# Kernel tuning notes

Hardware: AMD Instinct MI355X
Metric: run time of the kernel (lower is better)

Reference implementation:

```python
import jax, jax.numpy as jnp
import numpy as np

TOP_K = 2


def setup_inputs() -> dict:
    key = jax.random.key(0)
    k1, k2, k3, k4 = jax.random.split(key, 4)
    B, D, H, E = 16384, 1024, 1024, 8
    return {
        "x": jax.random.normal(k1, (B, D), dtype=jnp.float32),
        "Wv": jax.random.normal(k2, (E, D, H), dtype=jnp.float32),
        "Wg": jax.random.normal(k3, (E, D, H), dtype=jnp.float32),
        "gate_w": jax.random.normal(k4, (E, D), dtype=jnp.float32) * (1.0 / np.sqrt(D)),
        "gate_b": jnp.zeros((E,), dtype=jnp.float32),
    }


def reference(x, Wv, Wg, gate_w, gate_b):
    # Router: softmax over expert logits, then top-k selection.
    logits = x @ gate_w.T + gate_b                      # [B, E]
    probs = jax.nn.softmax(logits, axis=1)
    topk_scores, topk_idx = jax.lax.top_k(probs, TOP_K)  # [B, K]

    B, E = probs.shape
    # Scatter top-k scores into a dense [B, E] combine matrix (zeros elsewhere).
    combine = jnp.zeros((B, E), dtype=probs.dtype).at[
        jnp.arange(B)[:, None], topk_idx
    ].add(topk_scores)

    # Dense per-expert SwiGLU; combine matrix zeros out non-selected experts,
    # so the math matches the grouped-gemm top-k dispatch exactly.
    v = jnp.einsum("bd,edh->beh", x, Wv)                # [B, E, H]
    g = jnp.einsum("bd,edh->beh", x, Wg)                # [B, E, H]
    act = v * jax.nn.sigmoid(g)                         # SwiGLU-style gating
    return jnp.einsum("be,beh->bh", combine, act)       # weighted combine [B, H]
```

## Files before the change

### kernel.cpp

```cpp
#include <hip/hip_runtime.h>

#define D_DIM 1024
#define H_DIM 1024
#define E_NUM 8
#define BM 128
#define BN 128
#define BK 64
#define CAP 5120
#define RT_TOK 32

typedef __attribute__((ext_vector_type(8))) _Float16 h8v;
typedef __attribute__((ext_vector_type(4))) _Float16 h4v;
typedef __attribute__((ext_vector_type(4))) float f4v;

__device__ __forceinline__ unsigned short f2h(float f) {
  union { _Float16 h; unsigned short u; } c;
  c.h = (_Float16)f;
  return c.u;
}

__global__ void convert_x_kernel(const float4* __restrict__ x,
                                 unsigned short* __restrict__ xh, int n4) {
  int i = blockIdx.x * blockDim.x + threadIdx.x;
  if (i >= n4) return;
  float4 v = x[i];
  ushort4 o;
  o.x = f2h(v.x); o.y = f2h(v.y); o.z = f2h(v.z); o.w = f2h(v.w);
  *(ushort4*)(xh + (size_t)i * 4) = o;
}

__global__ void transpose_w_kernel(const float* __restrict__ W,
                                   unsigned short* __restrict__ Wt) {
  __shared__ float tile[32][33];
  int e = blockIdx.z;
  int h0 = blockIdx.x * 32, d0 = blockIdx.y * 32;
  const float* Wp = W + (size_t)e * D_DIM * H_DIM;
  unsigned short* Wtp = Wt + (size_t)e * H_DIM * D_DIM;
#pragma unroll
  for (int j = 0; j < 32; j += 8)
    tile[threadIdx.y + j][threadIdx.x] =
        Wp[(size_t)(d0 + threadIdx.y + j) * H_DIM + (h0 + threadIdx.x)];
  __syncthreads();
#pragma unroll
  for (int j = 0; j < 32; j += 8)
    Wtp[(size_t)(h0 + threadIdx.y + j) * D_DIM + (d0 + threadIdx.x)] =
        f2h(tile[threadIdx.x][threadIdx.y + j]);
}

__global__ __launch_bounds__(256) void router_kernel(
    const float4* __restrict__ x4, const float4* __restrict__ gw4,
    const float* __restrict__ gb, int* __restrict__ counts,
    int* __restrict__ bucket, float* __restrict__ scoreB,
    int* __restrict__ slotOf, int B) {
  __shared__ float4 gwS[E_NUM * 256];
  __shared__ short eSelS[RT_TOK][2];
  __shared__ float sSelS[RT_TOK][2];
  __shared__ int lCnt[E_NUM], lBase[E_NUM];
  __shared__ unsigned char lOff[RT_TOK][2];
  int tid = threadIdx.x;
  for (int i = tid; i < E_NUM * 256; i += 256) gwS[i] = gw4[i];
  if (tid < E_NUM) lCnt[tid] = 0;
  __syncthreads();
  int wid = tid >> 6, lane = tid & 63;
  for (int rep = 0; rep < RT_TOK / 4; rep++) {
    int t = wid * (RT_TOK / 4) + rep;
    int b = blockIdx.x * RT_TOK + t;
    float acc[E_NUM];
#pragma unroll
    for (int e = 0; e < E_NUM; e++) acc[e] = 0.0f;
#pragma unroll
    for (int i = 0; i < 4; i++) {
      float4 xv = x4[(size_t)b * 256 + i * 64 + lane];
#pragma unroll
      for (int e = 0; e < E_NUM; e++) {
        float4 w = gwS[e * 256 + i * 64 + lane];
        acc[e] += xv.x * w.x + xv.y * w.y + xv.z * w.z + xv.w * w.w;
      }
    }
#pragma unroll
    for (int e = 0; e < E_NUM; e++) {
#pragma unroll
      for (int off = 32; off > 0; off >>= 1) acc[e] += __shfl_down(acc[e], off);
    }
    if (lane == 0) {
      float l[E_NUM];
#pragma unroll
      for (int e = 0; e < E_NUM; e++) l[e] = acc[e] + gb[e];
      int i0 = 0;
#pragma unroll
      for (int e = 1; e < E_NUM; e++) if (l[e] > l[i0]) i0 = e;
      int i1 = (i0 == 0) ? 1 : 0;
#pragma unroll
      for (int e = 0; e < E_NUM; e++) if (e != i0 && l[e] > l[i1]) i1 = e;
      float mx = l[i0];
      float denom = 0.0f;
#pragma unroll
      for (int e = 0; e < E_NUM; e++) denom += __expf(l[e] - mx);
      eSelS[t][0] = (short)i0; sSelS[t][0] = 1.0f / denom;
      eSelS[t][1] = (short)i1; sSelS[t][1] = __expf(l[i1] - mx) / denom;
    }
  }
  __syncthreads();
  if (tid < RT_TOK) {
    lOff[tid][0] = (unsigned char)atomicAdd(&lCnt[eSelS[tid][0]], 1);
    lOff[tid][1] = (unsigned char)atomicAdd(&lCnt[eSelS[tid][1]], 1);
  }
  __syncthreads();
  if (tid < E_NUM) lBase[tid] = atomicAdd(&counts[tid * 32], lCnt[tid]);
  __syncthreads();
  if (tid < RT_TOK) {
    int b = blockIdx.x * RT_TOK + tid;
#pragma unroll
    for (int j = 0; j < 2; j++) {
      int e = eSelS[tid][j];
      int pos = lBase[e] + lOff[tid][j];
      if (pos < CAP) {
        int slot = e * CAP + pos;
        bucket[slot] = b;
        scoreB[slot] = sSelS[tid][j];
        slotOf[b * 2 + j] = slot;
      }
    }
  }
}

template <bool USE_PARTIAL>
__global__ __launch_bounds__(256, 2) void moe_gemm_kernel(
    const unsigned short* __restrict__ xh, const unsigned short* __restrict__ Wvt,
    const unsigned short* __restrict__ Wgt, const int* __restrict__ counts,
    const int* __restrict__ bucket, const float* __restrict__ scoreB,
    _Float16* __restrict__ partial, float* __restrict__ out, int B) {
  int e = blockIdx.z;
  int cnt = counts[e * 32];
  int m0 = blockIdx.x * BM;
  if (m0 >= cnt) return;
  int n0 = blockIdx.y * BN;

  __shared__ unsigned short As[BM * BK];
  __shared__ unsigned short Bvs[BN * BK];
  __shared__ unsigned short Bgs[BN * BK];
  __shared__ int tokS[BM];
  __shared__ float scS[BM];

  int tid = threadIdx.x;
  if (tid < BM) {
    int gr = m0 + tid;
    bool vld = gr < cnt;
    tokS[tid] = vld ? bucket[e * CAP + gr] : 0;
    scS[tid] = vld ? scoreB[e * CAP + gr] : 0.0f;
  }
  __syncthreads();

  int wid = tid >> 6, lane = tid & 63;
  int wm = wid & 1, wn = wid >> 1;
  int quad = lane >> 4, lr = lane & 15;

  f4v accv[4][4], accg[4][4];
#pragma unroll
  for (int a = 0; a < 4; a++)
#pragma unroll
    for (int bb = 0; bb < 4; bb++) {
      f4v z = {0.f, 0.f, 0.f, 0.f};
      accv[a][bb] = z;
      accg[a][bb] = z;
    }

  const unsigned short* Bv0 = Wvt + (size_t)(e * H_DIM + n0) * D_DIM;
  const unsigned short* Bg0 = Wgt + (size_t)(e * H_DIM + n0) * D_DIM;

  for (int kt = 0; kt < D_DIM / BK; kt++) {
    int k0 = kt * BK;
    uint4 va[4], vb[4], vg[4];
#pragma unroll
    for (int i = 0; i < 4; i++) {
      int id = tid + 256 * i;
      int row = id >> 3, c = id & 7;
      int tok = tokS[row];
      va[i] = *(const uint4*)(xh + (size_t)tok * D_DIM + k0 + c * 8);
      vb[i] = *(const uint4*)(Bv0 + (size_t)row * D_DIM + k0 + c * 8);
      vg[i] = *(const uint4*)(Bg0 + (size_t)row * D_DIM + k0 + c * 8);
    }
#pragma unroll
    for (int i = 0; i < 4; i++) {
      int id = tid + 256 * i;
      int row = id >> 3, c = id & 7;
      int off = row * BK + ((c ^ (row & 7)) * 8);
      *(uint4*)(As + off) = va[i];
      *(uint4*)(Bvs + off) = vb[i];
      *(uint4*)(Bgs + off) = vg[i];
    }
    __syncthreads();

    h8v af[4][2], bfr[4][2];
#pragma unroll
    for (int fm = 0; fm < 4; fm++)
#pragma unroll
      for (int s = 0; s < 2; s++) {
        int row = wm * 64 + fm * 16 + lr;
        int c = s * 4 + quad;
        af[fm][s] = *(const h8v*)(As + row * BK + ((c ^ (row & 7)) * 8));
      }
#pragma unroll
    for (int fn = 0; fn < 4; fn++)
#pragma unroll
      for (int s = 0; s < 2; s++) {
        int row = wn * 64 + fn * 16 + lr;
        int c = s * 4 + quad;
        bfr[fn][s] = *(const h8v*)(Bvs + row * BK + ((c ^ (row & 7)) * 8));
      }
#pragma unroll
    for (int fm = 0; fm < 4; fm++)
#pragma unroll
      for (int fn = 0; fn < 4; fn++)
#pragma unroll
        for (int s = 0; s < 2; s++)
          accv[fm][fn] = __builtin_amdgcn_mfma_f32_16x16x32_f16(
              af[fm][s], bfr[fn][s], accv[fm][fn], 0, 0, 0);
#pragma unroll
    for (int fn = 0; fn < 4; fn++)
#pragma unroll
      for (int s = 0; s < 2; s++) {
        int row = wn * 64 + fn * 16 + lr;
        int c = s * 4 + quad;
        bfr[fn][s] = *(const h8v*)(Bgs + row * BK + ((c ^ (row & 7)) * 8));
      }
#pragma unroll
    for (int fm = 0; fm < 4; fm++)
#pragma unroll
      for (int fn = 0; fn < 4; fn++)
#pragma unroll
        for (int s = 0; s < 2; s++)
          accg[fm][fn] = __builtin_amdgcn_mfma_f32_16x16x32_f16(
              af[fm][s], bfr[fn][s], accg[fm][fn], 0, 0, 0);
    __syncthreads();
  }

#pragma unroll
  for (int fm = 0; fm < 4; fm++) {
#pragma unroll
    for (int r = 0; r < 4; r++) {
      int row = wm * 64 + fm * 16 + quad * 4 + r;
      float sc = scS[row];
      if (USE_PARTIAL) {
        int slot = e * CAP + m0 + row;
        _Float16* pr = partial + (size_t)slot * H_DIM;
#pragma unroll
        for (int fn = 0; fn < 4; fn++) {
          int col = n0 + wn * 64 + fn * 16 + lr;
          float v = accv[fm][fn][r];
          float g = accg[fm][fn][r];
          pr[col] = (_Float16)(v * sc / (1.0f + __expf(-g)));
        }
      } else {
        int tok = tokS[row];
#pragma unroll
        for (int fn = 0; fn < 4; fn++) {
          int col = n0 + wn * 64 + fn * 16 + lr;
          float v = accv[fm][fn][r];
          float g = accg[fm][fn][r];
          atomicAdd(&out[(size_t)tok * H_DIM + col], v * sc / (1.0f + __expf(-g)));
        }
      }
    }
  }
}

__global__ __launch_bounds__(256) void gather_kernel(
    const _Float16* __restrict__ partial, const int* __restrict__ slotOf,
    float* __restrict__ out) {
  int b = blockIdx.x;
  int tid = threadIdx.x;
  int s0 = slotOf[b * 2], s1 = slotOf[b * 2 + 1];
  h4v a = ((const h4v*)(partial + (size_t)s0 * H_DIM))[tid];
  h4v c = ((const h4v*)(partial + (size_t)s1 * H_DIM))[tid];
  float4 o;
  o.x = (float)a[0] + (float)c[0];
  o.y = (float)a[1] + (float)c[1];
  o.z = (float)a[2] + (float)c[2];
  o.w = (float)a[3] + (float)c[3];
  ((float4*)(out + (size_t)b * H_DIM))[tid] = o;
}

extern "C" void kernel_launch(void* const* d_in, const int* in_sizes, int n_in,
                              void* d_out, int out_size, void* d_ws, size_t ws_size,
                              hipStream_t stream) {
  const float* x = (const float*)d_in[0];
  const float* Wv = (const float*)d_in[1];
  const float* Wg = (const float*)d_in[2];
  const float* gw = (const float*)d_in[3];
  const float* gb = (const float*)d_in[4];
  float* out = (float*)d_out;
  const int B = in_sizes[0] / D_DIM;

  char* ws = (char*)d_ws;
  unsigned short* xh = (unsigned short*)ws;
  size_t off = (size_t)B * D_DIM * 2;
  unsigned short* Wvt = (unsigned short*)(ws + off);
  off += (size_t)E_NUM * H_DIM * D_DIM * 2;
  unsigned short* Wgt = (unsigned short*)(ws + off);
  off += (size_t)E_NUM * H_DIM * D_DIM * 2;
  int* counts = (int*)(ws + off);
  off += 4096;
  int* bucket = (int*)(ws + off);
  off += (size_t)E_NUM * CAP * 4;
  float* scoreB = (float*)(ws + off);
  off += (size_t)E_NUM * CAP * 4;
  int* slotOf = (int*)(ws + off);
  off += (size_t)B * 2 * 4;
  _Float16* partial = (_Float16*)(ws + off);
  size_t need = off + (size_t)E_NUM * CAP * H_DIM * 2;
  bool use_partial = ws_size >= need;

  hipMemsetAsync(counts, 0, 4096, stream);
  if (!use_partial) hipMemsetAsync(d_out, 0, (size_t)out_size * 4, stream);

  int n4 = B * D_DIM / 4;
  convert_x_kernel<<<(n4 + 255) / 256, 256, 0, stream>>>((const float4*)x, xh, n4);
  transpose_w_kernel<<<dim3(H_DIM / 32, D_DIM / 32, E_NUM), dim3(32, 8), 0, stream>>>(Wv, Wvt);
  transpose_w_kernel<<<dim3(H_DIM / 32, D_DIM / 32, E_NUM), dim3(32, 8), 0, stream>>>(Wg, Wgt);
  router_kernel<<<B / RT_TOK, 256, 0, stream>>>(
      (const float4*)x, (const float4*)gw, gb, counts, bucket, scoreB, slotOf, B);
  if (use_partial) {
    moe_gemm_kernel<true><<<dim3(CAP / BM, H_DIM / BN, E_NUM), 256, 0, stream>>>(
        xh, Wvt, Wgt, counts, bucket, scoreB, partial, out, B);
    gather_kernel<<<B, 256, 0, stream>>>(partial, slotOf, out);
  } else {
    moe_gemm_kernel<false><<<dim3(CAP / BM, H_DIM / BN, E_NUM), 256, 0, stream>>>(
        xh, Wvt, Wgt, counts, bucket, scoreB, partial, out, B);
  }
}
```

Measured before the change: 390.6 us.

## Fuse x conversion into router, use direct global-to-LDS loads, widen transpose and gather

Measured after the change: 355.9 us. 8.9% less time.

```diff
diff --git a/kernel.cpp b/kernel.cpp
--- a/kernel.cpp
+++ b/kernel.cpp
@@ -10,7 +10,6 @@
 #define RT_TOK 32
 
 typedef __attribute__((ext_vector_type(8))) _Float16 h8v;
-typedef __attribute__((ext_vector_type(4))) _Float16 h4v;
 typedef __attribute__((ext_vector_type(4))) float f4v;
 
 __device__ __forceinline__ unsigned short f2h(float f) {
@@ -19,39 +18,51 @@
   return c.u;
 }
 
-__global__ void convert_x_kernel(const float4* __restrict__ x,
-                                 unsigned short* __restrict__ xh, int n4) {
-  int i = blockIdx.x * blockDim.x + threadIdx.x;
-  if (i >= n4) return;
-  float4 v = x[i];
-  ushort4 o;
-  o.x = f2h(v.x); o.y = f2h(v.y); o.z = f2h(v.z); o.w = f2h(v.w);
-  *(ushort4*)(xh + (size_t)i * 4) = o;
-}
-
-__global__ void transpose_w_kernel(const float* __restrict__ W,
-                                   unsigned short* __restrict__ Wt) {
-  __shared__ float tile[32][33];
-  int e = blockIdx.z;
-  int h0 = blockIdx.x * 32, d0 = blockIdx.y * 32;
+__device__ __forceinline__ void gl2lds16(const void* g, void* l) {
+  __builtin_amdgcn_global_load_lds(
+      (const __attribute__((address_space(1))) unsigned int*)g,
+      (__attribute__((address_space(3))) unsigned int*)l, 16, 0, 0);
+}
+
+__global__ __launch_bounds__(256) void transpose_w_kernel(
+    const float* __restrict__ Wv, const float* __restrict__ Wg,
+    unsigned short* __restrict__ Wvt, unsigned short* __restrict__ Wgt) {
+  __shared__ float tile[64][65];
+  int z = blockIdx.z;
+  const float* W = (z & 1) ? Wg : Wv;
+  unsigned short* Wt = (z & 1) ? Wgt : Wvt;
+  int e = z >> 1;
+  int h0 = blockIdx.x * 64, d0 = blockIdx.y * 64;
   const float* Wp = W + (size_t)e * D_DIM * H_DIM;
   unsigned short* Wtp = Wt + (size_t)e * H_DIM * D_DIM;
-#pragma unroll
-  for (int j = 0; j < 32; j += 8)
-    tile[threadIdx.y + j][threadIdx.x] =
-        Wp[(size_t)(d0 + threadIdx.y + j) * H_DIM + (h0 + threadIdx.x)];
-  __syncthreads();
-#pragma unroll
-  for (int j = 0; j < 32; j += 8)
-    Wtp[(size_t)(h0 + threadIdx.y + j) * D_DIM + (d0 + threadIdx.x)] =
-        f2h(tile[threadIdx.x][threadIdx.y + j]);
+  int t = threadIdx.x;
+#pragma unroll
+  for (int j = 0; j < 4; j++) {
+    int id = t + 256 * j;
+    int dd = id >> 4, hc = id & 15;
+    float4 v = *(const float4*)(Wp + (size_t)(d0 + dd) * H_DIM + h0 + hc * 4);
+    tile[dd][hc * 4 + 0] = v.x;
+    tile[dd][hc * 4 + 1] = v.y;
+    tile[dd][hc * 4 + 2] = v.z;
+    tile[dd][hc * 4 + 3] = v.w;
+  }
+  __syncthreads();
+#pragma unroll
+  for (int j = 0; j < 2; j++) {
+    int id = t + 256 * j;
+    int h_ = id >> 3, dc = id & 7;
+    unsigned short tmp[8];
+#pragma unroll
+    for (int k = 0; k < 8; k++) tmp[k] = f2h(tile[dc * 8 + k][h_]);
+    *(uint4*)(Wtp + (size_t)(h0 + h_) * D_DIM + d0 + dc * 8) = *(uint4*)tmp;
+  }
 }
 
 __global__ __launch_bounds__(256) void router_kernel(
     const float4* __restrict__ x4, const float4* __restrict__ gw4,
     const float* __restrict__ gb, int* __restrict__ counts,
     int* __restrict__ bucket, float* __restrict__ scoreB,
-    int* __restrict__ slotOf, int B) {
+    int* __restrict__ slotOf, ushort4* __restrict__ xh4, int B) {
   __shared__ float4 gwS[E_NUM * 256];
   __shared__ short eSelS[RT_TOK][2];
   __shared__ float sSelS[RT_TOK][2];
@@ -71,6 +82,9 @@
 #pragma unroll
     for (int i = 0; i < 4; i++) {
       float4 xv = x4[(size_t)b * 256 + i * 64 + lane];
+      ushort4 o;
+      o.x = f2h(xv.x); o.y = f2h(xv.y); o.z = f2h(xv.z); o.w = f2h(xv.w);
+      xh4[(size_t)b * 256 + i * 64 + lane] = o;
 #pragma unroll
       for (int e = 0; e < E_NUM; e++) {
         float4 w = gwS[e * 256 + i * 64 + lane];
@@ -155,6 +169,22 @@
   int wm = wid & 1, wn = wid >> 1;
   int quad = lane >> 4, lr = lane & 15;
 
+  const unsigned short* Bv0 = Wvt + (size_t)(e * H_DIM + n0) * D_DIM;
+  const unsigned short* Bg0 = Wgt + (size_t)(e * H_DIM + n0) * D_DIM;
+
+  int cswh = ((lane & 7) ^ (lane >> 3)) * 8;
+  const unsigned short *pA[4], *pBv[4], *pBg[4];
+  char *lD[4];
+#pragma unroll
+  for (int i = 0; i < 4; i++) {
+    int W = wid * 4 + i;
+    int row = W * 8 + (lane >> 3);
+    pA[i] = xh + (size_t)tokS[row] * D_DIM + cswh;
+    pBv[i] = Bv0 + (size_t)row * D_DIM + cswh;
+    pBg[i] = Bg0 + (size_t)row * D_DIM + cswh;
+    lD[i] = (char*)nullptr + W * 1024;
+  }
+
   f4v accv[4][4], accg[4][4];
 #pragma unroll
   for (int a = 0; a < 4; a++)
@@ -165,29 +195,14 @@
       accg[a][bb] = z;
     }
 
-  const unsigned short* Bv0 = Wvt + (size_t)(e * H_DIM + n0) * D_DIM;
-  const unsigned short* Bg0 = Wgt + (size_t)(e * H_DIM + n0) * D_DIM;
-
   for (int kt = 0; kt < D_DIM / BK; kt++) {
-    int k0 = kt * BK;
-    uint4 va[4], vb[4], vg[4];
 #pragma unroll
     for (int i = 0; i < 4; i++) {
-      int id = tid + 256 * i;
-      int row = id >> 3, c = id & 7;
-      int tok = tokS[row];
-      va[i] = *(const uint4*)(xh + (size_t)tok * D_DIM + k0 + c * 8);
-      vb[i] = *(const uint4*)(Bv0 + (size_t)row * D_DIM + k0 + c * 8);
-      vg[i] = *(const uint4*)(Bg0 + (size_t)row * D_DIM + k0 + c * 8);
-    }
-#pragma unroll
-    for (int i = 0; i < 4; i++) {
-      int id = tid + 256 * i;
-      int row = id >> 3, c = id & 7;
-      int off = row * BK + ((c ^ (row & 7)) * 8);
-      *(uint4*)(As + off) = va[i];
-      *(uint4*)(Bvs + off) = vb[i];
-      *(uint4*)(Bgs + off) = vg[i];
+      size_t w = (size_t)(lD[i] - (char*)nullptr);
+      gl2lds16(pA[i], (char*)As + w);
+      gl2lds16(pBv[i], (char*)Bvs + w);
+      gl2lds16(pBg[i], (char*)Bgs + w);
+      pA[i] += BK; pBv[i] += BK; pBg[i] += BK;
     }
     __syncthreads();
 
@@ -268,17 +283,25 @@
 __global__ __launch_bounds__(256) void gather_kernel(
     const _Float16* __restrict__ partial, const int* __restrict__ slotOf,
     float* __restrict__ out) {
-  int b = blockIdx.x;
-  int tid = threadIdx.x;
+  int b = blockIdx.x * 2 + (threadIdx.x >> 7);
+  int t = threadIdx.x & 127;
   int s0 = slotOf[b * 2], s1 = slotOf[b * 2 + 1];
-  h4v a = ((const h4v*)(partial + (size_t)s0 * H_DIM))[tid];
-  h4v c = ((const h4v*)(partial + (size_t)s1 * H_DIM))[tid];
-  float4 o;
-  o.x = (float)a[0] + (float)c[0];
-  o.y = (float)a[1] + (float)c[1];
-  o.z = (float)a[2] + (float)c[2];
-  o.w = (float)a[3] + (float)c[3];
-  ((float4*)(out + (size_t)b * H_DIM))[tid] = o;
+  if ((unsigned)s0 >= E_NUM * CAP) s0 = 0;
+  if ((unsigned)s1 >= E_NUM * CAP) s1 = 0;
+  h8v a = ((const h8v*)(partial + (size_t)s0 * H_DIM))[t];
+  h8v c = ((const h8v*)(partial + (size_t)s1 * H_DIM))[t];
+  float4 o0, o1;
+  o0.x = (float)a[0] + (float)c[0];
+  o0.y = (float)a[1] + (float)c[1];
+  o0.z = (float)a[2] + (float)c[2];
+  o0.w = (float)a[3] + (float)c[3];
+  o1.x = (float)a[4] + (float)c[4];
+  o1.y = (float)a[5] + (float)c[5];
+  o1.z = (float)a[6] + (float)c[6];
+  o1.w = (float)a[7] + (float)c[7];
+  float4* op = (float4*)(out + (size_t)b * H_DIM);
+  op[t * 2] = o0;
+  op[t * 2 + 1] = o1;
 }
 
 extern "C" void kernel_launch(void* const* d_in, const int* in_sizes, int n_in,
@@ -314,16 +337,15 @@
   hipMemsetAsync(counts, 0, 4096, stream);
   if (!use_partial) hipMemsetAsync(d_out, 0, (size_t)out_size * 4, stream);
 
-  int n4 = B * D_DIM / 4;
-  convert_x_kernel<<<(n4 + 255) / 256, 256, 0, stream>>>((const float4*)x, xh, n4);
-  transpose_w_kernel<<<dim3(H_DIM / 32, D_DIM / 32, E_NUM), dim3(32, 8), 0, stream>>>(Wv, Wvt);
-  transpose_w_kernel<<<dim3(H_DIM / 32, D_DIM / 32, E_NUM), dim3(32, 8), 0, stream>>>(Wg, Wgt);
   router_kernel<<<B / RT_TOK, 256, 0, stream>>>(
-      (const float4*)x, (const float4*)gw, gb, counts, bucket, scoreB, slotOf, B);
+      (const float4*)x, (const float4*)gw, gb, counts, bucket, scoreB, slotOf,
+      (ushort4*)xh, B);
+  transpose_w_kernel<<<dim3(H_DIM / 64, D_DIM / 64, 2 * E_NUM), 256, 0, stream>>>(
+      Wv, Wg, Wvt, Wgt);
   if (use_partial) {
     moe_gemm_kernel<true><<<dim3(CAP / BM, H_DIM / BN, E_NUM), 256, 0, stream>>>(
         xh, Wvt, Wgt, counts, bucket, scoreB, partial, out, B);
-    gather_kernel<<<B, 256, 0, stream>>>(partial, slotOf, out);
+    gather_kernel<<<B / 2, 256, 0, stream>>>(partial, slotOf, out);
   } else {
     moe_gemm_kernel<false><<<dim3(CAP / BM, H_DIM / BN, E_NUM), 256, 0, stream>>>(
         xh, Wvt, Wgt, counts, bucket, scoreB, partial, out, B);
```
